# Kernel optimization log

Hardware: AMD Instinct MI355X
Metric: run time of the kernel (lower is better)

Reference implementation:

```python
import jax, jax.numpy as jnp
import numpy as np
import math

B, S, D, H, L, V = 2, 2048, 1024, 16, 2, 32000
HD = D // H          # head_dim = 64
FF = 4 * D           # ffn hidden = 4096
NEG_INF = -1e9


def setup_inputs() -> dict:
    key = jax.random.key(0)
    ks = jax.random.split(key, 12)
    w = lambda k, shape: jax.random.normal(k, shape, dtype=jnp.float32) * 0.02
    return {
        "tokens": jax.random.randint(ks[0], (B, S), 0, V),
        "tok_emb": w(ks[1], (V, D)),
        "pos_emb": w(ks[2], (S, D)),
        # torch nn.Linear weights are [out, in]; stacked over layers
        "wq": w(ks[3], (L, D, D)),
        "wk": w(ks[4], (L, D, D)),
        "wv": w(ks[5], (L, D, D)),
        "wo": w(ks[6], (L, D, D)),
        "w1": w(ks[7], (L, FF, D)),
        "w2": w(ks[8], (L, D, FF)),
        "ln1_g": jnp.ones((L, D)), "ln1_b": jnp.zeros((L, D)),
        "ln2_g": jnp.ones((L, D)), "ln2_b": jnp.zeros((L, D)),
        "lnf_g": jnp.ones((D,)), "lnf_b": jnp.zeros((D,)),
        "w_out": w(ks[9], (V, D)),
    }


def _layernorm(x, g, b):
    m = jnp.mean(x, axis=-1, keepdims=True)
    v = jnp.mean(jnp.square(x - m), axis=-1, keepdims=True)
    return (x - m) * jax.lax.rsqrt(v + 1e-5) * g + b


def _transformer(tokens, tok_emb, pos_emb, wq, wk, wv, wo, w1, w2,
                 ln1_g, ln1_b, ln2_g, ln2_b, lnf_g, lnf_b, w_out):
    s = tokens.shape[1]
    # causal additive mask [1,1,S,S]
    mask = jnp.where(jnp.tril(jnp.ones((s, s), dtype=bool)), 0.0, NEG_INF)[None, None]
    h = tok_emb[tokens] + pos_emb[None, :s]
    scale = 1.0 / math.sqrt(HD)
    for l in range(L):
        # pre-norm attention
        a_in = _layernorm(h, ln1_g[l], ln1_b[l])
        q = (a_in @ wq[l].T).reshape(B, s, H, HD)
        k = (a_in @ wk[l].T).reshape(B, s, H, HD)
        v = (a_in @ wv[l].T).reshape(B, s, H, HD)
        scores = jnp.einsum('bqhd,bkhd->bhqk', q, k) * scale + mask
        attn = jax.nn.softmax(scores.astype(jnp.float32), axis=-1).astype(h.dtype)
        o = jnp.einsum('bhqk,bkhd->bqhd', attn, v).reshape(B, s, D)
        h = h + o @ wo[l].T
        # pre-norm ReLU FFN
        f_in = _layernorm(h, ln2_g[l], ln2_b[l])
        h = h + jax.nn.relu(f_in @ w1[l].T) @ w2[l].T
    h = _layernorm(h, lnf_g, lnf_b)
    return h @ w_out.T  # [B,S,V]


def reference(tokens, tok_emb, pos_emb, wq, wk, wv, wo, w1, w2,
              ln1_g, ln1_b, ln2_g, ln2_b, lnf_g, lnf_b, w_out):
    return _transformer(tokens, tok_emb, pos_emb, wq, wk, wv, wo, w1, w2,
                        ln1_g, ln1_b, ln2_g, ln2_b, lnf_g, lnf_b, w_out)
```

## Files before the change

### kernel.cpp

```cpp
#include <hip/hip_runtime.h>

#define Bv 2
#define Sv 2048
#define Dv 1024
#define Hv 16
#define HDv 64
#define FFv 4096
#define Vv 32000

typedef short bf16x8 __attribute__((ext_vector_type(8)));
typedef float f32x4 __attribute__((ext_vector_type(4)));
typedef unsigned short us8 __attribute__((ext_vector_type(8)));
typedef unsigned short us4 __attribute__((ext_vector_type(4)));
typedef unsigned short u16;

__device__ __forceinline__ u16 f2bf(float f) {
  union { float f; unsigned u; } x; x.f = f;
  x.u += 0x7fffu + ((x.u >> 16) & 1u);
  return (u16)(x.u >> 16);
}
__device__ __forceinline__ u16 f2bf_rtz(float f) {
  union { float f; unsigned u; } x; x.f = f;
  return (u16)(x.u >> 16);
}

__device__ __forceinline__ void gld16(const void* g, void* l) {
  __builtin_amdgcn_global_load_lds(
      (const __attribute__((address_space(1))) unsigned*)g,
      (__attribute__((address_space(3))) unsigned*)l, 16, 0, 0);
}

__global__ __launch_bounds__(256) void k_embed(const int* __restrict__ tok,
    const float* __restrict__ te, const float* __restrict__ pe,
    float* __restrict__ h) {
  int row = blockIdx.x;
  int s = row & (Sv - 1);
  int t = tok[row];
  float4 va = ((const float4*)(te + (size_t)t * Dv))[threadIdx.x];
  float4 vb = ((const float4*)(pe + (size_t)s * Dv))[threadIdx.x];
  float4 o;
  o.x = va.x + vb.x; o.y = va.y + vb.y; o.z = va.z + vb.z; o.w = va.w + vb.w;
  ((float4*)(h + (size_t)row * Dv))[threadIdx.x] = o;
}

__global__ __launch_bounds__(256) void k_cvt(const float* __restrict__ x,
    u16* __restrict__ y, int n4) {
  int i = blockIdx.x * 256 + threadIdx.x;
  if (i >= n4) return;
  float4 v = ((const float4*)x)[i];
  us4 o = { f2bf(v.x), f2bf(v.y), f2bf(v.z), f2bf(v.w) };
  ((us4*)y)[i] = o;
}

__global__ __launch_bounds__(256) void k_ln(const float* __restrict__ x,
    const float* __restrict__ g, const float* __restrict__ bb,
    u16* __restrict__ y) {
  int row = blockIdx.x, t = threadIdx.x;
  float4 v = ((const float4*)(x + (size_t)row * Dv))[t];
  float s = v.x + v.y + v.z + v.w;
#pragma unroll
  for (int m = 32; m; m >>= 1) s += __shfl_xor(s, m, 64);
  __shared__ float red[4];
  if ((t & 63) == 0) red[t >> 6] = s;
  __syncthreads();
  float mean = (red[0] + red[1] + red[2] + red[3]) * (1.0f / Dv);
  __syncthreads();
  float dx = v.x - mean, dy = v.y - mean, dz = v.z - mean, dw = v.w - mean;
  float s2 = dx * dx + dy * dy + dz * dz + dw * dw;
#pragma unroll
  for (int m = 32; m; m >>= 1) s2 += __shfl_xor(s2, m, 64);
  if ((t & 63) == 0) red[t >> 6] = s2;
  __syncthreads();
  float var = (red[0] + red[1] + red[2] + red[3]) * (1.0f / Dv);
  float rstd = rsqrtf(var + 1e-5f);
  float4 gg = ((const float4*)g)[t];
  float4 be = ((const float4*)bb)[t];
  us4 o = { f2bf(dx * rstd * gg.x + be.x), f2bf(dy * rstd * gg.y + be.y),
            f2bf(dz * rstd * gg.z + be.z), f2bf(dw * rstd * gg.w + be.w) };
  ((us4*)(y + (size_t)row * Dv))[t] = o;
}

__device__ __forceinline__ void stage32(const u16* __restrict__ g, int ldK,
    u16* lds, int row_base, int kt, int lane) {
  int row = row_base + (lane >> 2);
  int slot = (lane & 3) ^ ((row >> 1) & 3);
  const u16* src = g + (size_t)row * ldK + (kt << 5) + (slot << 3);
  gld16(src, lds + (row_base << 5));
}

__device__ __forceinline__ bf16x8 ldfragA(const u16* lds, int row, int ks) {
  return *(const bf16x8*)((const char*)lds + row * 64 + ((ks ^ ((row >> 1) & 3)) << 4));
}

template <int EPI>
__global__ __launch_bounds__(512, 4) void k_gemm8(const u16* __restrict__ A,
    const u16* __restrict__ Bm, const float* __restrict__ res,
    float* __restrict__ Cf, u16* __restrict__ Cb, int M, int N, int K) {
  __shared__ u16 As[2][128 * 32];
  __shared__ u16 Bs[2][256 * 32];
  int TM = M >> 7, TN = N >> 8, nwg = TM * TN;
  int orig = blockIdx.x;
  int qd = nwg >> 3, rm = nwg & 7, xcd = orig & 7;
  int wg = (xcd < rm ? xcd * (qd + 1) : rm * (qd + 1) + (xcd - rm) * qd) + (orig >> 3);
  int bm = wg % TM, bn = wg / TM;
  int m0 = bm << 7, n0 = bn << 8;
  int lane = threadIdx.x & 63, wid = threadIdx.x >> 6;
  int wr = wid >> 2, wc = wid & 3;
  int NT = K >> 5;
  const u16* Ag = A + (size_t)m0 * K;
  const u16* Bg = Bm + (size_t)n0 * K;
  int frow = lane & 15, ks = lane >> 4;

  f32x4 acc[4][4] = {};
  bf16x8 af[4], bf[4];

#pragma unroll
  for (int tt = 0; tt < 2; tt++) {
    stage32(Ag, K, As[tt], wid * 16, tt, lane);
    stage32(Bg, K, Bs[tt], wid * 32, tt, lane);
    stage32(Bg, K, Bs[tt], wid * 32 + 16, tt, lane);
  }
  asm volatile("s_waitcnt vmcnt(3)" ::: "memory");
  __builtin_amdgcn_s_barrier();

  for (int t = 0; t < NT; t++) {
    int p = t & 1;
    const u16* Ab = As[p];
    const u16* Bb = Bs[p];
#pragma unroll
    for (int f = 0; f < 4; f++) af[f] = ldfragA(Ab, wr * 64 + f * 16 + frow, ks);
#pragma unroll
    for (int n = 0; n < 4; n++) bf[n] = ldfragA(Bb, wc * 64 + n * 16 + frow, ks);
    __builtin_amdgcn_s_barrier();
    asm volatile("s_waitcnt lgkmcnt(0)" ::: "memory");
    __builtin_amdgcn_sched_barrier(0);
    __builtin_amdgcn_s_setprio(1);
#pragma unroll
    for (int f = 0; f < 2; f++)
#pragma unroll
      for (int n = 0; n < 4; n++)
        acc[f][n] = __builtin_amdgcn_mfma_f32_16x16x32_bf16(af[f], bf[n], acc[f][n], 0, 0, 0);
    __builtin_amdgcn_s_setprio(0);
    __builtin_amdgcn_sched_barrier(0);
    __builtin_amdgcn_s_barrier();
    if (t < NT - 2) {
      stage32(Ag, K, As[p], wid * 16, t + 2, lane);
      stage32(Bg, K, Bs[p], wid * 32, t + 2, lane);
      stage32(Bg, K, Bs[p], wid * 32 + 16, t + 2, lane);
    }
    __builtin_amdgcn_s_setprio(1);
#pragma unroll
    for (int f = 0; f < 2; f++)
#pragma unroll
      for (int n = 0; n < 4; n++)
        acc[2 + f][n] = __builtin_amdgcn_mfma_f32_16x16x32_bf16(af[2 + f], bf[n], acc[2 + f][n], 0, 0, 0);
    __builtin_amdgcn_s_setprio(0);
    __builtin_amdgcn_sched_barrier(0);
    if (t < NT - 2) { asm volatile("s_waitcnt vmcnt(3)" ::: "memory"); }
    else            { asm volatile("s_waitcnt vmcnt(0)" ::: "memory"); }
    __builtin_amdgcn_s_barrier();
  }

#pragma unroll
  for (int f = 0; f < 4; f++) {
#pragma unroll
    for (int r = 0; r < 4; r++) {
      int row = m0 + wr * 64 + f * 16 + (lane >> 4) * 4 + r;
#pragma unroll
      for (int n = 0; n < 4; n++) {
        int col = n0 + wc * 64 + n * 16 + frow;
        float val = acc[f][n][r];
        size_t idx = (size_t)row * N + col;
        if constexpr (EPI == 1) { Cf[idx] = val + res[idx]; }
        else if constexpr (EPI == 0) { __builtin_nontemporal_store(val, &Cf[idx]); }
        else if constexpr (EPI == 2) { Cb[idx] = f2bf(val); }
        else { Cb[idx] = f2bf(fmaxf(val, 0.0f)); }
      }
    }
  }
}

template <int EPI>
__global__ __launch_bounds__(256, 4) void k_gemmv(const u16* __restrict__ A,
    const u16* __restrict__ Bm, const float* __restrict__ res,
    float* __restrict__ Cf, u16* __restrict__ Cb, int M, int N, int K) {
  __shared__ u16 As[2][128 * 32];
  __shared__ u16 Bs[2][128 * 32];
  int TM = M >> 7, TN = N >> 7, nwg = TM * TN;
  int orig = blockIdx.x;
  int qd = nwg >> 3, rm = nwg & 7, xcd = orig & 7;
  int wg = (xcd < rm ? xcd * (qd + 1) : rm * (qd + 1) + (xcd - rm) * qd) + (orig >> 3);
  int bm = wg % TM, bn = wg / TM;
  int m0 = bm << 7, n0 = bn << 7;
  int lane = threadIdx.x & 63, wid = threadIdx.x >> 6;
  int wr = wid >> 1, wc = wid & 1;
  int NT = K >> 5;
  const u16* Ag = A + (size_t)m0 * K;
  const u16* Bg = Bm + (size_t)n0 * K;
  int frow = lane & 15, ks = lane >> 4;

  f32x4 acc[4][4] = {};
  bf16x8 af[4], bf[4];

#pragma unroll
  for (int tt = 0; tt < 2; tt++) {
    stage32(Ag, K, As[tt], wid * 32, tt, lane);
    stage32(Ag, K, As[tt], wid * 32 + 16, tt, lane);
    stage32(Bg, K, Bs[tt], wid * 32, tt, lane);
    stage32(Bg, K, Bs[tt], wid * 32 + 16, tt, lane);
  }
  asm volatile("s_waitcnt vmcnt(4)" ::: "memory");
  __builtin_amdgcn_s_barrier();

  for (int t = 0; t < NT; t++) {
    int p = t & 1;
    const u16* Ab = As[p];
    const u16* Bb = Bs[p];
#pragma unroll
    for (int f = 0; f < 4; f++) af[f] = ldfragA(Ab, wr * 64 + f * 16 + frow, ks);
#pragma unroll
    for (int n = 0; n < 4; n++) bf[n] = ldfragA(Bb, wc * 64 + n * 16 + frow, ks);
    __builtin_amdgcn_s_barrier();
    asm volatile("s_waitcnt lgkmcnt(0)" ::: "memory");
    __builtin_amdgcn_sched_barrier(0);
    __builtin_amdgcn_s_setprio(1);
#pragma unroll
    for (int f = 0; f < 2; f++)
#pragma unroll
      for (int n = 0; n < 4; n++)
        acc[f][n] = __builtin_amdgcn_mfma_f32_16x16x32_bf16(af[f], bf[n], acc[f][n], 0, 0, 0);
    __builtin_amdgcn_s_setprio(0);
    __builtin_amdgcn_sched_barrier(0);
    __builtin_amdgcn_s_barrier();
    if (t < NT - 2) {
      stage32(Ag, K, As[p], wid * 32, t + 2, lane);
      stage32(Ag, K, As[p], wid * 32 + 16, t + 2, lane);
      stage32(Bg, K, Bs[p], wid * 32, t + 2, lane);
      stage32(Bg, K, Bs[p], wid * 32 + 16, t + 2, lane);
    }
    __builtin_amdgcn_s_setprio(1);
#pragma unroll
    for (int f = 0; f < 2; f++)
#pragma unroll
      for (int n = 0; n < 4; n++)
        acc[2 + f][n] = __builtin_amdgcn_mfma_f32_16x16x32_bf16(af[2 + f], bf[n], acc[2 + f][n], 0, 0, 0);
    __builtin_amdgcn_s_setprio(0);
    __builtin_amdgcn_sched_barrier(0);
    if (t < NT - 2) { asm volatile("s_waitcnt vmcnt(4)" ::: "memory"); }
    else            { asm volatile("s_waitcnt vmcnt(0)" ::: "memory"); }
    __builtin_amdgcn_s_barrier();
  }

#pragma unroll
  for (int f = 0; f < 4; f++) {
#pragma unroll
    for (int r = 0; r < 4; r++) {
      int row = m0 + wr * 64 + f * 16 + (lane >> 4) * 4 + r;
#pragma unroll
      for (int n = 0; n < 4; n++) {
        int col = n0 + wc * 64 + n * 16 + frow;
        float val = acc[f][n][r];
        size_t idx = (size_t)row * N + col;
        if constexpr (EPI == 1) { Cf[idx] = val + res[idx]; }
        else if constexpr (EPI == 0) { __builtin_nontemporal_store(val, &Cf[idx]); }
        else if constexpr (EPI == 2) { Cb[idx] = f2bf(val); }
        else { Cb[idx] = f2bf(fmaxf(val, 0.0f)); }
      }
    }
  }
}

__global__ __launch_bounds__(256) void k_transpose(const u16* __restrict__ v,
    u16* __restrict__ vt, int stride) {
  int st = blockIdx.x & 31;
  int bh = blockIdx.x >> 5;
  int b = bh >> 4, hh = bh & 15;
  __shared__ u16 tile[64][72];
  int t = threadIdx.x;
  int rr = t >> 3, cc = (t & 7) << 3;
#pragma unroll
  for (int it = 0; it < 2; it++) {
    int r = rr + it * 32;
    us8 val = *(const us8*)(v + (size_t)(b * Sv + st * 64 + r) * stride + hh * HDv + cc);
    *(us8*)&tile[r][cc] = val;
  }
  __syncthreads();
#pragma unroll
  for (int it = 0; it < 2; it++) {
    int d = rr + it * 32;
    us8 val;
#pragma unroll
    for (int j = 0; j < 8; j++) val[j] = tile[cc + j][d];
    *(us8*)(vt + ((size_t)bh * HDv + d) * Sv + st * 64 + cc) = val;
  }
}

__global__ __launch_bounds__(256) void k_attn(const u16* __restrict__ qg,
    const u16* __restrict__ kg, const u16* __restrict__ vt,
    u16* __restrict__ og) {
  int qt = blockIdx.x & 15;
  int bh = blockIdx.x >> 4;
  int b = bh >> 4, hh = bh & 15;
  int wv = threadIdx.x >> 6, lane = threadIdx.x & 63;
  int q0 = qt * 128 + wv * 32;
  __shared__ u16 plds_s[4][32 * 40];
  __shared__ float alds_s[4][2][16];
  u16* plds = plds_s[wv];
  float (*alds)[16] = alds_s[wv];
  const int QS = 3 * Dv;
  const float scale = 0.125f;
  int qcol = lane & 15, g = lane >> 4;

  bf16x8 qf[2][2];
#pragma unroll
  for (int fm = 0; fm < 2; fm++)
#pragma unroll
    for (int dh = 0; dh < 2; dh++)
      qf[fm][dh] = *(const bf16x8*)(qg + (size_t)(b * Sv + q0 + fm * 16 + qcol) * QS
                                    + hh * HDv + dh * 32 + g * 8);

  f32x4 oacc[2][4] = {};
  float mrun[2] = { -1e30f, -1e30f };
  float lrun[2] = { 0.0f, 0.0f };

  int ktmax = (q0 + 31) >> 5;
  for (int kt = 0; kt <= ktmax; kt++) {
    int k0 = kt * 32;
    bf16x8 kf[2][2];
#pragma unroll
    for (int kn = 0; kn < 2; kn++)
#pragma unroll
      for (int dh = 0; dh < 2; dh++)
        kf[kn][dh] = *(const bf16x8*)(kg + (size_t)(b * Sv + k0 + kn * 16 + qcol) * QS
                                      + hh * HDv + dh * 32 + g * 8);
    f32x4 sa[2][2] = {};
#pragma unroll
    for (int dh = 0; dh < 2; dh++)
#pragma unroll
      for (int fm = 0; fm < 2; fm++)
#pragma unroll
        for (int kn = 0; kn < 2; kn++)
          sa[fm][kn] = __builtin_amdgcn_mfma_f32_16x16x32_bf16(kf[kn][dh], qf[fm][dh], sa[fm][kn], 0, 0, 0);

    bool full = (k0 + 31 <= q0);
#pragma unroll
    for (int fm = 0; fm < 2; fm++) {
      int qrow = q0 + fm * 16 + qcol;
      float s[2][4];
#pragma unroll
      for (int kn = 0; kn < 2; kn++)
#pragma unroll
        for (int r = 0; r < 4; r++) {
          float v = sa[fm][kn][r] * scale;
          if (!full && (k0 + kn * 16 + g * 4 + r) > qrow) v = -1e30f;
          s[kn][r] = v;
        }
      float rmx = s[0][0];
#pragma unroll
      for (int kn = 0; kn < 2; kn++)
#pragma unroll
        for (int r = 0; r < 4; r++) rmx = fmaxf(rmx, s[kn][r]);
      rmx = fmaxf(rmx, __shfl_xor(rmx, 16, 64));
      rmx = fmaxf(rmx, __shfl_xor(rmx, 32, 64));
      float nm;
      if (__all(rmx - mrun[fm] <= 8.0f)) {
        nm = mrun[fm];
      } else {
        nm = fmaxf(mrun[fm], rmx);
        float alpha = __expf(mrun[fm] - nm);
        mrun[fm] = nm;
        lrun[fm] *= alpha;
        if (g == 0) alds[fm][qcol] = alpha;
#pragma unroll
        for (int r = 0; r < 4; r++) {
          float al = alds[fm][g * 4 + r];
#pragma unroll
          for (int dn = 0; dn < 4; dn++) oacc[fm][dn][r] *= al;
        }
      }
      float rs = 0.0f;
      float pv[2][4];
#pragma unroll
      for (int kn = 0; kn < 2; kn++)
#pragma unroll
        for (int r = 0; r < 4; r++) { pv[kn][r] = __expf(s[kn][r] - nm); rs += pv[kn][r]; }
      rs += __shfl_xor(rs, 16, 64);
      rs += __shfl_xor(rs, 32, 64);
      lrun[fm] += rs;
#pragma unroll
      for (int kn = 0; kn < 2; kn++) {
        us4 pk = { f2bf_rtz(pv[kn][0]), f2bf_rtz(pv[kn][1]),
                   f2bf_rtz(pv[kn][2]), f2bf_rtz(pv[kn][3]) };
        *(us4*)(plds + (fm * 16 + qcol) * 40 + kn * 16 + g * 4) = pk;
      }
    }
    bf16x8 pf[2];
#pragma unroll
    for (int fm = 0; fm < 2; fm++)
      pf[fm] = *(const bf16x8*)(plds + (fm * 16 + qcol) * 40 + g * 8);
    bf16x8 vf[4];
#pragma unroll
    for (int dn = 0; dn < 4; dn++)
      vf[dn] = *(const bf16x8*)(vt + ((size_t)bh * HDv + dn * 16 + qcol) * Sv
                                + k0 + g * 8);
#pragma unroll
    for (int fm = 0; fm < 2; fm++)
#pragma unroll
      for (int dn = 0; dn < 4; dn++)
        oacc[fm][dn] = __builtin_amdgcn_mfma_f32_16x16x32_bf16(pf[fm], vf[dn], oacc[fm][dn], 0, 0, 0);
  }

#pragma unroll
  for (int fm = 0; fm < 2; fm++)
    if (g == 0) alds[fm][qcol] = 1.0f / lrun[fm];
#pragma unroll
  for (int fm = 0; fm < 2; fm++)
#pragma unroll
    for (int r = 0; r < 4; r++) {
      float li = alds[fm][g * 4 + r];
      int row = q0 + fm * 16 + g * 4 + r;
#pragma unroll
      for (int dn = 0; dn < 4; dn++)
        og[(size_t)(b * Sv + row) * Dv + hh * HDv + dn * 16 + qcol] =
            f2bf(oacc[fm][dn][r] * li);
    }
}

extern "C" void kernel_launch(void* const* d_in, const int* in_sizes, int n_in,
                              void* d_out, int out_size, void* d_ws, size_t ws_size,
                              hipStream_t stream) {
  const int*   tok  = (const int*)d_in[0];
  const float* te   = (const float*)d_in[1];
  const float* pe   = (const float*)d_in[2];
  const float* wq   = (const float*)d_in[3];
  const float* wk   = (const float*)d_in[4];
  const float* wvv  = (const float*)d_in[5];
  const float* wo   = (const float*)d_in[6];
  const float* w1   = (const float*)d_in[7];
  const float* w2   = (const float*)d_in[8];
  const float* ln1g = (const float*)d_in[9];
  const float* ln1b = (const float*)d_in[10];
  const float* ln2g = (const float*)d_in[11];
  const float* ln2b = (const float*)d_in[12];
  const float* lnfg = (const float*)d_in[13];
  const float* lnfb = (const float*)d_in[14];
  const float* wout = (const float*)d_in[15];
  float* out = (float*)d_out;

  char* p = (char*)d_ws;
  float* h  = (float*)p; p += (size_t)4096 * 1024 * 4;
  u16* a    = (u16*)p;   p += (size_t)4096 * 1024 * 2;
  u16* qkv  = (u16*)p;   p += (size_t)4096 * 3072 * 2;
  u16* vt   = (u16*)p;   p += (size_t)32 * 64 * 2048 * 2;
  u16* o    = (u16*)p;   p += (size_t)4096 * 1024 * 2;
  u16* f1   = (u16*)p;   p += (size_t)4096 * 4096 * 2;
  u16* wb   = (u16*)p;   p += (size_t)32000 * 1024 * 2;

  const int M = Bv * Sv;

  k_embed<<<M, 256, 0, stream>>>(tok, te, pe, h);
  for (int l = 0; l < 2; l++) {
    k_ln<<<M, 256, 0, stream>>>(h, ln1g + l * Dv, ln1b + l * Dv, a);
    k_cvt<<<1024, 256, 0, stream>>>(wq  + (size_t)l * Dv * Dv, wb,              (Dv * Dv) / 4);
    k_cvt<<<1024, 256, 0, stream>>>(wk  + (size_t)l * Dv * Dv, wb + Dv * Dv,    (Dv * Dv) / 4);
    k_cvt<<<1024, 256, 0, stream>>>(wvv + (size_t)l * Dv * Dv, wb + 2 * Dv * Dv,(Dv * Dv) / 4);
    k_gemm8<2><<<32 * 12, 512, 0, stream>>>(a, wb, nullptr, nullptr, qkv, M, 3 * Dv, Dv);
    k_transpose<<<1024, 256, 0, stream>>>(qkv + 2 * Dv, vt, 3 * Dv);
    k_attn<<<512, 256, 0, stream>>>(qkv, qkv + Dv, vt, o);
    k_cvt<<<1024, 256, 0, stream>>>(wo + (size_t)l * Dv * Dv, wb, (Dv * Dv) / 4);
    k_gemmv<1><<<32 * 8, 256, 0, stream>>>(o, wb, h, h, nullptr, M, Dv, Dv);
    k_ln<<<M, 256, 0, stream>>>(h, ln2g + l * Dv, ln2b + l * Dv, a);
    k_cvt<<<4096, 256, 0, stream>>>(w1 + (size_t)l * FFv * Dv, wb, (FFv * Dv) / 4);
    k_gemm8<3><<<32 * 16, 512, 0, stream>>>(a, wb, nullptr, nullptr, f1, M, FFv, Dv);
    k_cvt<<<4096, 256, 0, stream>>>(w2 + (size_t)l * Dv * FFv, wb, (Dv * FFv) / 4);
    k_gemmv<1><<<32 * 8, 256, 0, stream>>>(f1, wb, h, h, nullptr, M, Dv, FFv);
  }
  k_ln<<<M, 256, 0, stream>>>(h, lnfg, lnfb, a);
  k_cvt<<<32000, 256, 0, stream>>>(wout, wb, (Vv * Dv) / 4);
  k_gemm8<0><<<32 * 125, 512, 0, stream>>>(a, wb, nullptr, out, nullptr, M, Vv, Dv);
}
```

Before: 995.6 us.

## Add 256x256x64 tiled GEMM kernel for FFN-up and vocab projection

Adds a new bf16 MFMA GEMM kernel with 256x256 output tiles, 64-wide K steps, a double-buffered LDS stage with an XOR swizzle, and a phased fragment-load/MFMA schedule using priority hints and sched barriers. It replaces the 128x256 kernel for the FFN first projection and the large vocabulary output GEMM. Larger tiles raise arithmetic intensity and cut global reloads of the A and B operands. In exchange the kernel uses 128KB of LDS per workgroup, has fewer workgroups, and needs more accumulator registers, which lowers occupancy and can cause wave-quantization or tail effects.

```diff
diff --git a/kernel.cpp b/kernel.cpp
--- a/kernel.cpp
+++ b/kernel.cpp
@@ -87,9 +87,146 @@
   const u16* src = g + (size_t)row * ldK + (kt << 5) + (slot << 3);
   gld16(src, lds + (row_base << 5));
 }
-
 __device__ __forceinline__ bf16x8 ldfragA(const u16* lds, int row, int ks) {
   return *(const bf16x8*)((const char*)lds + row * 64 + ((ks ^ ((row >> 1) & 3)) << 4));
+}
+
+__device__ __forceinline__ void stage64(const u16* __restrict__ g, int ldK,
+    u16* lds, int row_base, int kt, int lane) {
+  int row = row_base + (lane >> 3);
+  int slot = (lane & 7) ^ (row & 7);
+  const u16* src = g + (size_t)row * ldK + (kt << 6) + (slot << 3);
+  gld16(src, lds + (row_base << 6));
+}
+__device__ __forceinline__ bf16x8 ldf64(const u16* lds, int row, int slot) {
+  return *(const bf16x8*)((const char*)lds + row * 128 + ((slot ^ (row & 7)) << 4));
+}
+
+template <int EPI>
+__global__ __launch_bounds__(512, 2) void k_256(const u16* __restrict__ A,
+    const u16* __restrict__ Bm, const float* __restrict__ res,
+    float* __restrict__ Cf, u16* __restrict__ Cb, int M, int N, int K) {
+  __shared__ u16 As[2][256 * 64];
+  __shared__ u16 Bs[2][256 * 64];
+  int TM = M >> 8, TN = N >> 8, nwg = TM * TN;
+  int orig = blockIdx.x;
+  int qd = nwg >> 3, rm = nwg & 7, xcd = orig & 7;
+  int wg = (xcd < rm ? xcd * (qd + 1) : rm * (qd + 1) + (xcd - rm) * qd) + (orig >> 3);
+  int bm = wg % TM, bn = wg / TM;
+  int m0 = bm << 8, n0 = bn << 8;
+  int lane = threadIdx.x & 63, wid = threadIdx.x >> 6;
+  int wr = wid >> 2, wc = wid & 3;
+  int NT = K >> 6;
+  const u16* Ag = A + (size_t)m0 * K;
+  const u16* Bg = Bm + (size_t)n0 * K;
+  int frow = lane & 15, ks = lane >> 4;
+
+  f32x4 acc[8][4] = {};
+  bf16x8 af[4], bk0[4], bk1[4];
+
+#pragma unroll
+  for (int tt = 0; tt < 2; tt++) {
+#pragma unroll
+    for (int j = 0; j < 4; j++) stage64(Ag, K, As[tt], wid * 32 + j * 8, tt, lane);
+#pragma unroll
+    for (int j = 0; j < 4; j++) stage64(Bg, K, Bs[tt], wid * 32 + j * 8, tt, lane);
+  }
+  asm volatile("s_waitcnt vmcnt(8)" ::: "memory");
+  __builtin_amdgcn_s_barrier();
+
+  for (int t = 0; t < NT; t++) {
+    int p = t & 1;
+    const u16* Ab = As[p];
+    const u16* Bb = Bs[p];
+#pragma unroll
+    for (int f = 0; f < 4; f++) af[f] = ldf64(Ab, wr * 128 + f * 16 + frow, ks);
+#pragma unroll
+    for (int n = 0; n < 4; n++) bk0[n] = ldf64(Bb, wc * 64 + n * 16 + frow, ks);
+    __builtin_amdgcn_s_barrier();
+    asm volatile("s_waitcnt lgkmcnt(0)" ::: "memory");
+    __builtin_amdgcn_sched_barrier(0);
+    __builtin_amdgcn_s_setprio(1);
+#pragma unroll
+    for (int f = 0; f < 4; f++)
+#pragma unroll
+      for (int n = 0; n < 4; n++)
+        acc[f][n] = __builtin_amdgcn_mfma_f32_16x16x32_bf16(af[f], bk0[n], acc[f][n], 0, 0, 0);
+    __builtin_amdgcn_s_setprio(0);
+    __builtin_amdgcn_sched_barrier(0);
+    __builtin_amdgcn_s_barrier();
+#pragma unroll
+    for (int f = 0; f < 4; f++) af[f] = ldf64(Ab, wr * 128 + 64 + f * 16 + frow, ks);
+#pragma unroll
+    for (int n = 0; n < 4; n++) bk1[n] = ldf64(Bb, wc * 64 + n * 16 + frow, 4 + ks);
+    __builtin_amdgcn_s_barrier();
+    asm volatile("s_waitcnt lgkmcnt(0)" ::: "memory");
+    __builtin_amdgcn_sched_barrier(0);
+    __builtin_amdgcn_s_setprio(1);
+#pragma unroll
+    for (int f = 0; f < 4; f++)
+#pragma unroll
+      for (int n = 0; n < 4; n++)
+        acc[4 + f][n] = __builtin_amdgcn_mfma_f32_16x16x32_bf16(af[f], bk0[n], acc[4 + f][n], 0, 0, 0);
+    __builtin_amdgcn_s_setprio(0);
+    __builtin_amdgcn_sched_barrier(0);
+    __builtin_amdgcn_s_barrier();
+#pragma unroll
+    for (int f = 0; f < 4; f++) af[f] = ldf64(Ab, wr * 128 + f * 16 + frow, 4 + ks);
+    __builtin_amdgcn_s_barrier();
+    asm volatile("s_waitcnt lgkmcnt(0)" ::: "memory");
+    __builtin_amdgcn_sched_barrier(0);
+    __builtin_amdgcn_s_setprio(1);
+#pragma unroll
+    for (int f = 0; f < 4; f++)
+#pragma unroll
+      for (int n = 0; n < 4; n++)
+        acc[f][n] = __builtin_amdgcn_mfma_f32_16x16x32_bf16(af[f], bk1[n], acc[f][n], 0, 0, 0);
+    __builtin_amdgcn_s_setprio(0);
+    __builtin_amdgcn_sched_barrier(0);
+    __builtin_amdgcn_s_barrier();
+#pragma unroll
+    for (int f = 0; f < 4; f++) af[f] = ldf64(Ab, wr * 128 + 64 + f * 16 + frow, 4 + ks);
+    __builtin_amdgcn_s_barrier();
+    asm volatile("s_waitcnt lgkmcnt(0)" ::: "memory");
+    __builtin_amdgcn_sched_barrier(0);
+    __builtin_amdgcn_s_setprio(1);
+#pragma unroll
+    for (int f = 0; f < 4; f++)
+#pragma unroll
+      for (int n = 0; n < 4; n++)
+        acc[4 + f][n] = __builtin_amdgcn_mfma_f32_16x16x32_bf16(af[f], bk1[n], acc[4 + f][n], 0, 0, 0);
+    __builtin_amdgcn_s_setprio(0);
+    __builtin_amdgcn_sched_barrier(0);
+    __builtin_amdgcn_s_barrier();
+    if (t + 2 < NT) {
+#pragma unroll
+      for (int j = 0; j < 4; j++) stage64(Ag, K, As[p], wid * 32 + j * 8, t + 2, lane);
+#pragma unroll
+      for (int j = 0; j < 4; j++) stage64(Bg, K, Bs[p], wid * 32 + j * 8, t + 2, lane);
+      asm volatile("s_waitcnt vmcnt(8)" ::: "memory");
+    } else {
+      asm volatile("s_waitcnt vmcnt(0)" ::: "memory");
+    }
+    __builtin_amdgcn_s_barrier();
+  }
+
+#pragma unroll
+  for (int f = 0; f < 8; f++) {
+#pragma unroll
+    for (int r = 0; r < 4; r++) {
+      int row = m0 + wr * 128 + f * 16 + (lane >> 4) * 4 + r;
+#pragma unroll
+      for (int n = 0; n < 4; n++) {
+        int col = n0 + wc * 64 + n * 16 + frow;
+        float val = acc[f][n][r];
+        size_t idx = (size_t)row * N + col;
+        if constexpr (EPI == 1) { Cf[idx] = val + res[idx]; }
+        else if constexpr (EPI == 0) { __builtin_nontemporal_store(val, &Cf[idx]); }
+        else if constexpr (EPI == 2) { Cb[idx] = f2bf(val); }
+        else { Cb[idx] = f2bf(fmaxf(val, 0.0f)); }
+      }
+    }
+  }
 }
 
 template <int EPI>
@@ -471,11 +608,11 @@
     k_gemmv<1><<<32 * 8, 256, 0, stream>>>(o, wb, h, h, nullptr, M, Dv, Dv);
     k_ln<<<M, 256, 0, stream>>>(h, ln2g + l * Dv, ln2b + l * Dv, a);
     k_cvt<<<4096, 256, 0, stream>>>(w1 + (size_t)l * FFv * Dv, wb, (FFv * Dv) / 4);
-    k_gemm8<3><<<32 * 16, 512, 0, stream>>>(a, wb, nullptr, nullptr, f1, M, FFv, Dv);
+    k_256<3><<<16 * 16, 512, 0, stream>>>(a, wb, nullptr, nullptr, f1, M, FFv, Dv);
     k_cvt<<<4096, 256, 0, stream>>>(w2 + (size_t)l * Dv * FFv, wb, (Dv * FFv) / 4);
     k_gemmv<1><<<32 * 8, 256, 0, stream>>>(f1, wb, h, h, nullptr, M, Dv, FFv);
   }
   k_ln<<<M, 256, 0, stream>>>(h, lnfg, lnfb, a);
   k_cvt<<<32000, 256, 0, stream>>>(wout, wb, (Vv * Dv) / 4);
-  k_gemm8<0><<<32 * 125, 512, 0, stream>>>(a, wb, nullptr, out, nullptr, M, Vv, Dv);
-}
+  k_256<0><<<16 * 125, 512, 0, stream>>>(a, wb, nullptr, out, nullptr, M, Vv, Dv);
+}
```

Result: slower. 1.075 ms (+8.0%).
